# Kernel optimization log

Measured on AMD Instinct MI355X. Metric: run time of the kernel, lower is better.

The kernel has to match this reference:

```python
import jax, jax.numpy as jnp
import numpy as np

H = 16  # n_head

def _rms_norm(x):
    eps = jnp.asarray(jnp.finfo(x.dtype).eps, x.dtype)
    ms = jnp.mean(jnp.square(x), axis=-1, keepdims=True)
    return x * jax.lax.rsqrt(ms + eps)

def _interp(x, pos):
    # x: [B,T,H,Dh]; pos: [B,T,H,Dh] float positions along axis 1
    T = x.shape[1]
    pos_floor = jnp.floor(pos)
    pos0 = jnp.clip(pos_floor, 0, T - 1).astype(jnp.int32)
    pos1 = jnp.clip(pos0 + 1, 0, T - 1)
    frac = pos - pos_floor
    x0 = jnp.take_along_axis(x, pos0, axis=1)
    x1 = jnp.take_along_axis(x, pos1, axis=1)
    return x0 + (x1 - x0) * frac

def setup_inputs() -> dict:
    key = jax.random.key(0)
    ks = jax.random.split(key, 5)
    B, T, D = 4, 4096, 2048
    x = jax.random.normal(ks[0], (B, T, D), dtype=jnp.float32)
    scale = 0.02
    Wq = jax.random.normal(ks[1], (D, D), dtype=jnp.float32) * scale
    Wk = jax.random.normal(ks[2], (D, D), dtype=jnp.float32) * scale
    Wsq = jax.random.normal(ks[3], (D, D), dtype=jnp.float32) * scale
    Wsk = jax.random.normal(ks[4], (D, D), dtype=jnp.float32) * scale
    return {"x": x, "Wq": Wq, "Wk": Wk, "Wsq": Wsq, "Wsk": Wsk}

def reference(x, Wq, Wk, Wsq, Wsk):
    B, T, D = x.shape
    Dh = D // H
    # projections (Linear with weight [out,in]: y = x @ W.T)
    q = _rms_norm((x @ Wq.T).reshape(B, T, H, Dh))
    k = _rms_norm((x @ Wk.T).reshape(B, T, H, Dh))
    sq = jax.nn.softplus(x @ Wsq.T).reshape(B, T, H, Dh)
    sk = jax.nn.softplus(x @ Wsk.T).reshape(B, T, H, Dh)
    t_idx = jnp.arange(T, dtype=x.dtype).reshape(1, T, 1, 1)
    posq = jnp.minimum(jnp.maximum(t_idx - sq, 0.0), t_idx)
    posk = jnp.minimum(jnp.maximum(t_idx - sk, 0.0), t_idx)
    q_def = _interp(q, posq)
    k_def = _interp(k, posk)
    return (q_def * k_def).reshape(B, T, D)
```

## Files before the change

kernel.cpp:

```cpp
#include <hip/hip_runtime.h>

typedef unsigned short u16;
typedef __bf16 bf16x8 __attribute__((ext_vector_type(8)));
typedef unsigned short u16x8 __attribute__((ext_vector_type(8)));
typedef unsigned short u16x4 __attribute__((ext_vector_type(4)));
typedef float f32x4 __attribute__((ext_vector_type(4)));

#define K_DIM 2048
#define BM 128
#define BN 128
#define BK 32

#define GLL16(g, l) __builtin_amdgcn_global_load_lds( \
    (const __attribute__((address_space(1))) void*)(g), \
    (__attribute__((address_space(3))) void*)(l), 16, 0, 0)

__device__ __forceinline__ u16 f2bf(float f) {
    unsigned int u = __builtin_bit_cast(unsigned int, f);
    u = (u + 0x7fffu + ((u >> 16) & 1u)) >> 16;
    return (u16)u;
}
__device__ __forceinline__ float bf2f(u16 h) {
    unsigned int u = ((unsigned int)h) << 16;
    return __builtin_bit_cast(float, u);
}
__device__ __forceinline__ float softplus_f(float v) {
    return fmaxf(v, 0.0f) + log1pf(expf(-fabsf(v)));
}

__global__ void pack_kernel(const float* __restrict__ src, u16* __restrict__ dst, int n4) {
    int i = blockIdx.x * blockDim.x + threadIdx.x;
    if (i >= n4) return;
    float4 v = ((const float4*)src)[i];
    u16x4 o;
    o[0] = f2bf(v.x); o[1] = f2bf(v.y); o[2] = f2bf(v.z); o[3] = f2bf(v.w);
    ((u16x4*)dst)[i] = o;
}

__global__ void pack4_kernel(const float* __restrict__ s0, const float* __restrict__ s1,
                             const float* __restrict__ s2, const float* __restrict__ s3,
                             u16* __restrict__ dst) {
    int i = blockIdx.x * blockDim.x + threadIdx.x;
    const float* src = (blockIdx.y == 0) ? s0 : (blockIdx.y == 1) ? s1
                     : (blockIdx.y == 2) ? s2 : s3;
    float4 v = ((const float4*)src)[i];
    u16x4 o;
    o[0] = f2bf(v.x); o[1] = f2bf(v.y); o[2] = f2bf(v.z); o[3] = f2bf(v.w);
    ((u16x4*)(dst + (size_t)blockIdx.y * 4194304))[i] = o;
}

__global__ __launch_bounds__(256) void gemm_fused(
    const u16* __restrict__ xb, const u16* __restrict__ wb,
    u16* __restrict__ qb, u16* __restrict__ kb,
    u16* __restrict__ sqb, u16* __restrict__ skb)
{
    __shared__ u16 Als[BM * BK];
    __shared__ u16 Bls[BM * BK];
    __shared__ float ss[BM];

    const int tid  = threadIdx.x;
    const int lane = tid & 63;
    const int wave = tid >> 6;
    const int wm = wave >> 1;
    const int wn = wave & 1;
    const int gm0 = blockIdx.y * BM;
    const int gn0 = blockIdx.x * BN;

    const int r0 = tid >> 2;
    const int qs = ((tid & 3) - ((tid >> 3) & 3)) & 3;
    const int kc = qs * 8;
    const u16* gA0 = xb + (size_t)(gm0 + r0) * K_DIM + kc;
    const u16* gA1 = gA0 + (size_t)64 * K_DIM;
    const u16* gB0 = wb + (size_t)(gn0 + r0) * K_DIM + kc;
    const u16* gB1 = gB0 + (size_t)64 * K_DIM;
    char* lA0 = (char*)Als + wave * 1024;
    char* lA1 = (char*)Als + 4096 + wave * 1024;
    char* lB0 = (char*)Bls + wave * 1024;
    char* lB1 = (char*)Bls + 4096 + wave * 1024;

    f32x4 acc[4][4] = {};

    const int mr = lane & 15;
    const int q  = lane >> 4;
    const int s  = (q + (mr >> 1)) & 3;
    const int fragoff = mr * 32 + s * 8;

    for (int kt = 0; kt < K_DIM / BK; ++kt) {
        GLL16(gA0, lA0); GLL16(gA1, lA1);
        GLL16(gB0, lB0); GLL16(gB1, lB1);
        gA0 += BK; gA1 += BK; gB0 += BK; gB1 += BK;
        __syncthreads();

        bf16x8 a[4], b[4];
#pragma unroll
        for (int i = 0; i < 4; ++i)
            a[i] = __builtin_bit_cast(bf16x8, *(const u16x8*)&Als[(wm * 4 + i) * 512 + fragoff]);
#pragma unroll
        for (int j = 0; j < 4; ++j)
            b[j] = __builtin_bit_cast(bf16x8, *(const u16x8*)&Bls[(wn * 4 + j) * 512 + fragoff]);
#pragma unroll
        for (int i = 0; i < 4; ++i)
#pragma unroll
            for (int j = 0; j < 4; ++j)
                acc[i][j] = __builtin_amdgcn_mfma_f32_16x16x32_bf16(a[i], b[j], acc[i][j], 0, 0, 0);
        __syncthreads();
    }

    const int which = gn0 >> 11;
    if (tid < BM) ss[tid] = 0.0f;
    __syncthreads();

    const int mbase = wm * 64 + (lane >> 4) * 4;
    const int col0  = (gn0 & 2047) + wn * 64 + (lane & 15);

    if (which < 2) {
#pragma unroll
        for (int i = 0; i < 4; ++i) {
#pragma unroll
            for (int r = 0; r < 4; ++r) {
                float sv = acc[i][0][r] * acc[i][0][r] + acc[i][1][r] * acc[i][1][r]
                         + acc[i][2][r] * acc[i][2][r] + acc[i][3][r] * acc[i][3][r];
                sv += __shfl_xor(sv, 1, 64);
                sv += __shfl_xor(sv, 2, 64);
                sv += __shfl_xor(sv, 4, 64);
                sv += __shfl_xor(sv, 8, 64);
                if ((lane & 15) == 0) atomicAdd(&ss[mbase + i * 16 + r], sv);
            }
        }
        __syncthreads();
    }

    u16* ob = (which == 0) ? qb : (which == 1) ? kb : (which == 2) ? sqb : skb;
#pragma unroll
    for (int i = 0; i < 4; ++i) {
#pragma unroll
        for (int r = 0; r < 4; ++r) {
            int m = mbase + i * 16 + r;
            size_t rowbase = (size_t)(gm0 + m) * 2048;
            float scale = 1.0f;
            if (which < 2)
                scale = rsqrtf(ss[m] * (1.0f / 128.0f) + 1.1920929e-07f);
#pragma unroll
            for (int j = 0; j < 4; ++j) {
                float v = acc[i][j][r];
                v = (which < 2) ? v * scale : softplus_f(v);
                ob[rowbase + col0 + j * 16] = f2bf(v);
            }
        }
    }
}

__global__ void interp_mul(const u16* __restrict__ qb, const u16* __restrict__ kb,
                           const u16* __restrict__ sqb, const u16* __restrict__ skb,
                           float* __restrict__ out)
{
    size_t base = ((size_t)blockIdx.x * 256 + threadIdx.x) * 8;
    int c0 = (int)(base & 2047);
    size_t bt = base >> 11;
    int t = (int)(bt & 4095);
    float tf = (float)t;
    size_t rb = (base >> 23) << 23;

    u16x8 sqv8 = *(const u16x8*)&sqb[base];
    u16x8 skv8 = *(const u16x8*)&skb[base];

    float o[8];
#pragma unroll
    for (int e = 0; e < 8; ++e) {
        float sqv = bf2f(sqv8[e]);
        float skv = bf2f(skv8[e]);
        float pq = fminf(fmaxf(tf - sqv, 0.0f), tf);
        float pk = fminf(fmaxf(tf - skv, 0.0f), tf);
        float pqf = floorf(pq), pkf = floorf(pk);
        int q0i = (int)pqf, k0i = (int)pkf;
        int q1i = min(q0i + 1, 4095), k1i = min(k0i + 1, 4095);
        float fq = pq - pqf, fk = pk - pkf;
        size_t oo = rb + (size_t)(c0 + e);
        float q0 = bf2f(qb[oo + ((size_t)q0i << 11)]);
        float q1 = bf2f(qb[oo + ((size_t)q1i << 11)]);
        float k0 = bf2f(kb[oo + ((size_t)k0i << 11)]);
        float k1 = bf2f(kb[oo + ((size_t)k1i << 11)]);
        float qd = q0 + (q1 - q0) * fq;
        float kd = k0 + (k1 - k0) * fk;
        o[e] = qd * kd;
    }
    float4 lo = make_float4(o[0], o[1], o[2], o[3]);
    float4 hi = make_float4(o[4], o[5], o[6], o[7]);
    float4* op = (float4*)&out[base];
    op[0] = lo;
    op[1] = hi;
}

extern "C" void kernel_launch(void* const* d_in, const int* in_sizes, int n_in,
                              void* d_out, int out_size, void* d_ws, size_t ws_size,
                              hipStream_t stream) {
    const float* x   = (const float*)d_in[0];
    const float* Wq  = (const float*)d_in[1];
    const float* Wk  = (const float*)d_in[2];
    const float* Wsq = (const float*)d_in[3];
    const float* Wsk = (const float*)d_in[4];
    float* out = (float*)d_out;

    const size_t NEED = 369098752;
    if (ws_size < NEED) return;
    char* ws = (char*)d_ws;
    u16* xb  = (u16*)(ws);
    u16* wb  = (u16*)(ws + 67108864);
    u16* qb  = (u16*)(ws + 100663296);
    u16* kb  = (u16*)(ws + 167772160);
    u16* sqb = (u16*)(ws + 234881024);
    u16* skb = (u16*)(ws + 301989888);

    pack_kernel<<<32768, 256, 0, stream>>>(x, xb, 8388608);
    dim3 wgrid(4096, 4);
    pack4_kernel<<<wgrid, 256, 0, stream>>>(Wq, Wk, Wsq, Wsk, wb);

    dim3 ggrid(64, 128);
    gemm_fused<<<ggrid, 256, 0, stream>>>(xb, wb, qb, kb, sqb, skb);

    interp_mul<<<16384, 256, 0, stream>>>(qb, kb, sqb, skb, out);
}
```

Before: 1.201 ms.

## Rewrite GEMM as 256x256 tile, 8-wave, double-buffered pipeline with phased MFMA scheduling

The fused projection GEMM moves from 128x128 tiles with 4 waves and a single-buffered BK=32 loop to 256x256 tiles with 8 waves. It double-buffers 64-wide K slices in LDS and issues the global-to-LDS loads in halves interleaved with MFMA phases. Explicit sched barriers, s_barrier, s_setprio and vmcnt waits overlap memory traffic with matrix math and raise data reuse per tile. In exchange it uses much more LDS and accumulator registers, and each block's RMS-norm reduction now spans two heads in the shared buffer.

```diff
diff --git a/kernel.cpp b/kernel.cpp
--- a/kernel.cpp
+++ b/kernel.cpp
@@ -7,13 +7,17 @@
 typedef float f32x4 __attribute__((ext_vector_type(4)));
 
 #define K_DIM 2048
-#define BM 128
-#define BN 128
-#define BK 32
 
 #define GLL16(g, l) __builtin_amdgcn_global_load_lds( \
     (const __attribute__((address_space(1))) void*)(g), \
     (__attribute__((address_space(3))) void*)(l), 16, 0, 0)
+
+#define SB()  __builtin_amdgcn_sched_barrier(0)
+#define BAR() __builtin_amdgcn_s_barrier()
+#define PH_PRE()  do { SB(); BAR(); SB(); } while (0)
+#define PH_END()  do { SB(); BAR(); SB(); } while (0)
+#define PH_END_V4() do { SB(); asm volatile("s_waitcnt vmcnt(4)"); SB(); BAR(); SB(); } while (0)
+#define MFMA_(av, bv, cc) (cc) = __builtin_amdgcn_mfma_f32_16x16x32_bf16((av), (bv), (cc), 0, 0, 0)
 
 __device__ __forceinline__ u16 f2bf(float f) {
     unsigned int u = __builtin_bit_cast(unsigned int, f);
@@ -49,73 +53,210 @@
     ((u16x4*)(dst + (size_t)blockIdx.y * 4194304))[i] = o;
 }
 
-__global__ __launch_bounds__(256) void gemm_fused(
+__global__ __launch_bounds__(512, 2) void gemm_fused(
     const u16* __restrict__ xb, const u16* __restrict__ wb,
     u16* __restrict__ qb, u16* __restrict__ kb,
     u16* __restrict__ sqb, u16* __restrict__ skb)
 {
-    __shared__ u16 Als[BM * BK];
-    __shared__ u16 Bls[BM * BK];
-    __shared__ float ss[BM];
+    __shared__ __align__(16) u16 Als[32768];
+    __shared__ __align__(16) u16 Bls[32768];
+    __shared__ float ss[512];
 
     const int tid  = threadIdx.x;
     const int lane = tid & 63;
     const int wave = tid >> 6;
-    const int wm = wave >> 1;
-    const int wn = wave & 1;
-    const int gm0 = blockIdx.y * BM;
-    const int gn0 = blockIdx.x * BN;
-
-    const int r0 = tid >> 2;
-    const int qs = ((tid & 3) - ((tid >> 3) & 3)) & 3;
-    const int kc = qs * 8;
-    const u16* gA0 = xb + (size_t)(gm0 + r0) * K_DIM + kc;
-    const u16* gA1 = gA0 + (size_t)64 * K_DIM;
-    const u16* gB0 = wb + (size_t)(gn0 + r0) * K_DIM + kc;
-    const u16* gB1 = gB0 + (size_t)64 * K_DIM;
-    char* lA0 = (char*)Als + wave * 1024;
-    char* lA1 = (char*)Als + 4096 + wave * 1024;
-    char* lB0 = (char*)Bls + wave * 1024;
-    char* lB1 = (char*)Bls + 4096 + wave * 1024;
-
-    f32x4 acc[4][4] = {};
-
-    const int mr = lane & 15;
-    const int q  = lane >> 4;
-    const int s  = (q + (mr >> 1)) & 3;
-    const int fragoff = mr * 32 + s * 8;
-
-    for (int kt = 0; kt < K_DIM / BK; ++kt) {
-        GLL16(gA0, lA0); GLL16(gA1, lA1);
-        GLL16(gB0, lB0); GLL16(gB1, lB1);
-        gA0 += BK; gA1 += BK; gB0 += BK; gB1 += BK;
-        __syncthreads();
-
-        bf16x8 a[4], b[4];
-#pragma unroll
-        for (int i = 0; i < 4; ++i)
-            a[i] = __builtin_bit_cast(bf16x8, *(const u16x8*)&Als[(wm * 4 + i) * 512 + fragoff]);
-#pragma unroll
-        for (int j = 0; j < 4; ++j)
-            b[j] = __builtin_bit_cast(bf16x8, *(const u16x8*)&Bls[(wn * 4 + j) * 512 + fragoff]);
-#pragma unroll
-        for (int i = 0; i < 4; ++i)
-#pragma unroll
-            for (int j = 0; j < 4; ++j)
-                acc[i][j] = __builtin_amdgcn_mfma_f32_16x16x32_bf16(a[i], b[j], acc[i][j], 0, 0, 0);
-        __syncthreads();
+    const int wm   = wave >> 2;
+    const int wn   = wave & 3;
+    const int gm0  = blockIdx.y * 256;
+    const int gn0  = blockIdx.x * 256;
+
+    const int q8 = (((lane & 3) - ((lane >> 3) & 3)) & 3) * 8;
+    const int sB = wave * 512;
+    const u16* pa0 = xb + (size_t)(gm0 + wave * 16 + (lane >> 2)) * K_DIM + q8;
+    const u16* pb0 = wb + (size_t)(gn0 + wave * 16 + (lane >> 2)) * K_DIM + q8;
+    const size_t SRC1 = (size_t)128 * K_DIM;
+
+    const int mr  = lane & 15;
+    const int srd = ((lane >> 4) + (mr >> 1)) & 3;
+    const int fro = mr * 32 + srd * 8;
+    const int aRB = wm * 8 * 512 + fro;
+    const int bRB = wn * 4 * 512 + fro;
+
+    f32x4 acc[8][4] = {};
+
+#define LDA(buf, i, ks) __builtin_bit_cast(bf16x8, *(const u16x8*)&Als[(buf)*16384 + (ks)*8192 + aRB + (i)*512])
+#define LDB(buf, j, ks) __builtin_bit_cast(bf16x8, *(const u16x8*)&Bls[(buf)*16384 + (ks)*8192 + bRB + (j)*512])
+#define STAGE_A(coff, dbase) do { \
+    GLL16(pa0 + (coff),          &Als[(dbase) + sB]); \
+    GLL16(pa0 + (coff) + SRC1,   &Als[(dbase) + sB + 4096]); \
+    GLL16(pa0 + (coff) + 32,     &Als[(dbase) + sB + 8192]); \
+    GLL16(pa0 + (coff) + SRC1 + 32, &Als[(dbase) + sB + 12288]); } while (0)
+#define STAGE_B(coff, dbase) do { \
+    GLL16(pb0 + (coff),          &Bls[(dbase) + sB]); \
+    GLL16(pb0 + (coff) + SRC1,   &Bls[(dbase) + sB + 4096]); \
+    GLL16(pb0 + (coff) + 32,     &Bls[(dbase) + sB + 8192]); \
+    GLL16(pb0 + (coff) + SRC1 + 32, &Bls[(dbase) + sB + 12288]); } while (0)
+#define STAGE_A_H0(coff, dbase) do { \
+    GLL16(pa0 + (coff),        &Als[(dbase) + sB]); \
+    GLL16(pa0 + (coff) + SRC1, &Als[(dbase) + sB + 4096]); } while (0)
+#define STAGE_A_H1(coff, dbase) do { \
+    GLL16(pa0 + (coff) + 32,        &Als[(dbase) + sB + 8192]); \
+    GLL16(pa0 + (coff) + SRC1 + 32, &Als[(dbase) + sB + 12288]); } while (0)
+#define STAGE_B_H0(coff, dbase) do { \
+    GLL16(pb0 + (coff),        &Bls[(dbase) + sB]); \
+    GLL16(pb0 + (coff) + SRC1, &Bls[(dbase) + sB + 4096]); } while (0)
+#define STAGE_B_H1(coff, dbase) do { \
+    GLL16(pb0 + (coff) + 32,        &Bls[(dbase) + sB + 8192]); \
+    GLL16(pb0 + (coff) + SRC1 + 32, &Bls[(dbase) + sB + 12288]); } while (0)
+
+    STAGE_A(0, 0);
+    STAGE_B(0, 0);
+    STAGE_B(64, 16384);
+    __syncthreads();
+
+    for (int it = 0; it < 16; ++it) {
+        bf16x8 aF[4][2], b01[2][2], b23[2][2];
+
+#pragma unroll
+        for (int i = 0; i < 4; ++i) { aF[i][0] = LDA(0, i, 0); aF[i][1] = LDA(0, i, 1); }
+#pragma unroll
+        for (int j = 0; j < 2; ++j) { b01[j][0] = LDB(0, j, 0); b01[j][1] = LDB(0, j, 1); }
+        STAGE_A_H0(64, 16384);
+        PH_PRE();
+        __builtin_amdgcn_s_setprio(1);
+#pragma unroll
+        for (int i = 0; i < 4; ++i) MFMA_(aF[i][0], b01[0][0], acc[i][0]);
+#pragma unroll
+        for (int i = 0; i < 4; ++i) MFMA_(aF[i][0], b01[1][0], acc[i][1]);
+#pragma unroll
+        for (int i = 0; i < 4; ++i) MFMA_(aF[i][1], b01[0][1], acc[i][0]);
+#pragma unroll
+        for (int i = 0; i < 4; ++i) MFMA_(aF[i][1], b01[1][1], acc[i][1]);
+        __builtin_amdgcn_s_setprio(0);
+        PH_END();
+
+#pragma unroll
+        for (int j = 0; j < 2; ++j) { b23[j][0] = LDB(0, j + 2, 0); b23[j][1] = LDB(0, j + 2, 1); }
+        STAGE_A_H1(64, 16384);
+        PH_PRE();
+        __builtin_amdgcn_s_setprio(1);
+#pragma unroll
+        for (int i = 0; i < 4; ++i) MFMA_(aF[i][0], b23[0][0], acc[i][2]);
+#pragma unroll
+        for (int i = 0; i < 4; ++i) MFMA_(aF[i][0], b23[1][0], acc[i][3]);
+#pragma unroll
+        for (int i = 0; i < 4; ++i) MFMA_(aF[i][1], b23[0][1], acc[i][2]);
+#pragma unroll
+        for (int i = 0; i < 4; ++i) MFMA_(aF[i][1], b23[1][1], acc[i][3]);
+        __builtin_amdgcn_s_setprio(0);
+        PH_END();
+
+#pragma unroll
+        for (int i = 0; i < 4; ++i) { aF[i][0] = LDA(0, i + 4, 0); aF[i][1] = LDA(0, i + 4, 1); }
+        STAGE_B_H0(128, 0);
+        PH_PRE();
+        __builtin_amdgcn_s_setprio(1);
+#pragma unroll
+        for (int i = 0; i < 4; ++i) MFMA_(aF[i][0], b23[0][0], acc[4 + i][2]);
+#pragma unroll
+        for (int i = 0; i < 4; ++i) MFMA_(aF[i][0], b23[1][0], acc[4 + i][3]);
+#pragma unroll
+        for (int i = 0; i < 4; ++i) MFMA_(aF[i][1], b23[0][1], acc[4 + i][2]);
+#pragma unroll
+        for (int i = 0; i < 4; ++i) MFMA_(aF[i][1], b23[1][1], acc[4 + i][3]);
+        __builtin_amdgcn_s_setprio(0);
+        PH_END();
+
+        STAGE_B_H1(128, 0);
+        PH_PRE();
+        __builtin_amdgcn_s_setprio(1);
+#pragma unroll
+        for (int i = 0; i < 4; ++i) MFMA_(aF[i][0], b01[0][0], acc[4 + i][0]);
+#pragma unroll
+        for (int i = 0; i < 4; ++i) MFMA_(aF[i][0], b01[1][0], acc[4 + i][1]);
+#pragma unroll
+        for (int i = 0; i < 4; ++i) MFMA_(aF[i][1], b01[0][1], acc[4 + i][0]);
+#pragma unroll
+        for (int i = 0; i < 4; ++i) MFMA_(aF[i][1], b01[1][1], acc[4 + i][1]);
+        __builtin_amdgcn_s_setprio(0);
+        PH_END_V4();
+
+#pragma unroll
+        for (int i = 0; i < 4; ++i) { aF[i][0] = LDA(1, i, 0); aF[i][1] = LDA(1, i, 1); }
+#pragma unroll
+        for (int j = 0; j < 2; ++j) { b01[j][0] = LDB(1, j, 0); b01[j][1] = LDB(1, j, 1); }
+        STAGE_A_H0(128, 0);
+        PH_PRE();
+        __builtin_amdgcn_s_setprio(1);
+#pragma unroll
+        for (int i = 0; i < 4; ++i) MFMA_(aF[i][0], b01[0][0], acc[i][0]);
+#pragma unroll
+        for (int i = 0; i < 4; ++i) MFMA_(aF[i][0], b01[1][0], acc[i][1]);
+#pragma unroll
+        for (int i = 0; i < 4; ++i) MFMA_(aF[i][1], b01[0][1], acc[i][0]);
+#pragma unroll
+        for (int i = 0; i < 4; ++i) MFMA_(aF[i][1], b01[1][1], acc[i][1]);
+        __builtin_amdgcn_s_setprio(0);
+        PH_END();
+
+#pragma unroll
+        for (int j = 0; j < 2; ++j) { b23[j][0] = LDB(1, j + 2, 0); b23[j][1] = LDB(1, j + 2, 1); }
+        STAGE_A_H1(128, 0);
+        PH_PRE();
+        __builtin_amdgcn_s_setprio(1);
+#pragma unroll
+        for (int i = 0; i < 4; ++i) MFMA_(aF[i][0], b23[0][0], acc[i][2]);
+#pragma unroll
+        for (int i = 0; i < 4; ++i) MFMA_(aF[i][0], b23[1][0], acc[i][3]);
+#pragma unroll
+        for (int i = 0; i < 4; ++i) MFMA_(aF[i][1], b23[0][1], acc[i][2]);
+#pragma unroll
+        for (int i = 0; i < 4; ++i) MFMA_(aF[i][1], b23[1][1], acc[i][3]);
+        __builtin_amdgcn_s_setprio(0);
+        PH_END();
+
+#pragma unroll
+        for (int i = 0; i < 4; ++i) { aF[i][0] = LDA(1, i + 4, 0); aF[i][1] = LDA(1, i + 4, 1); }
+        STAGE_B_H0(192, 16384);
+        PH_PRE();
+        __builtin_amdgcn_s_setprio(1);
+#pragma unroll
+        for (int i = 0; i < 4; ++i) MFMA_(aF[i][0], b23[0][0], acc[4 + i][2]);
+#pragma unroll
+        for (int i = 0; i < 4; ++i) MFMA_(aF[i][0], b23[1][0], acc[4 + i][3]);
+#pragma unroll
+        for (int i = 0; i < 4; ++i) MFMA_(aF[i][1], b23[0][1], acc[4 + i][2]);
+#pragma unroll
+        for (int i = 0; i < 4; ++i) MFMA_(aF[i][1], b23[1][1], acc[4 + i][3]);
+        __builtin_amdgcn_s_setprio(0);
+        PH_END();
+
+        STAGE_B_H1(192, 16384);
+        PH_PRE();
+        __builtin_amdgcn_s_setprio(1);
+#pragma unroll
+        for (int i = 0; i < 4; ++i) MFMA_(aF[i][0], b01[0][0], acc[4 + i][0]);
+#pragma unroll
+        for (int i = 0; i < 4; ++i) MFMA_(aF[i][0], b01[1][0], acc[4 + i][1]);
+#pragma unroll
+        for (int i = 0; i < 4; ++i) MFMA_(aF[i][1], b01[0][1], acc[4 + i][0]);
+#pragma unroll
+        for (int i = 0; i < 4; ++i) MFMA_(aF[i][1], b01[1][1], acc[4 + i][1]);
+        __builtin_amdgcn_s_setprio(0);
+        PH_END_V4();
+
+        pa0 += 128; pb0 += 128;
     }
+    asm volatile("s_waitcnt vmcnt(0)" ::: "memory");
 
     const int which = gn0 >> 11;
-    if (tid < BM) ss[tid] = 0.0f;
+    ss[tid] = 0.0f;
     __syncthreads();
 
-    const int mbase = wm * 64 + (lane >> 4) * 4;
-    const int col0  = (gn0 & 2047) + wn * 64 + (lane & 15);
-
+    const int h = wn >> 1;
     if (which < 2) {
 #pragma unroll
-        for (int i = 0; i < 4; ++i) {
+        for (int i = 0; i < 8; ++i) {
 #pragma unroll
             for (int r = 0; r < 4; ++r) {
                 float sv = acc[i][0][r] * acc[i][0][r] + acc[i][1][r] * acc[i][1][r]
@@ -124,22 +265,24 @@
                 sv += __shfl_xor(sv, 2, 64);
                 sv += __shfl_xor(sv, 4, 64);
                 sv += __shfl_xor(sv, 8, 64);
-                if ((lane & 15) == 0) atomicAdd(&ss[mbase + i * 16 + r], sv);
+                if ((lane & 15) == 0)
+                    atomicAdd(&ss[h * 256 + wm * 128 + i * 16 + (lane >> 4) * 4 + r], sv);
             }
         }
         __syncthreads();
     }
 
     u16* ob = (which == 0) ? qb : (which == 1) ? kb : (which == 2) ? sqb : skb;
-#pragma unroll
-    for (int i = 0; i < 4; ++i) {
+    const int col0 = (gn0 & 2047) + wn * 64 + (lane & 15);
+#pragma unroll
+    for (int i = 0; i < 8; ++i) {
 #pragma unroll
         for (int r = 0; r < 4; ++r) {
-            int m = mbase + i * 16 + r;
-            size_t rowbase = (size_t)(gm0 + m) * 2048;
+            const int m = wm * 128 + i * 16 + (lane >> 4) * 4 + r;
+            const size_t rowbase = (size_t)(gm0 + m) * 2048;
             float scale = 1.0f;
             if (which < 2)
-                scale = rsqrtf(ss[m] * (1.0f / 128.0f) + 1.1920929e-07f);
+                scale = rsqrtf(ss[h * 256 + m] * (1.0f / 128.0f) + 1.1920929e-07f);
 #pragma unroll
             for (int j = 0; j < 4; ++j) {
                 float v = acc[i][j][r];
@@ -184,11 +327,9 @@
         float kd = k0 + (k1 - k0) * fk;
         o[e] = qd * kd;
     }
-    float4 lo = make_float4(o[0], o[1], o[2], o[3]);
-    float4 hi = make_float4(o[4], o[5], o[6], o[7]);
     float4* op = (float4*)&out[base];
-    op[0] = lo;
-    op[1] = hi;
+    op[0] = make_float4(o[0], o[1], o[2], o[3]);
+    op[1] = make_float4(o[4], o[5], o[6], o[7]);
 }
 
 extern "C" void kernel_launch(void* const* d_in, const int* in_sizes, int n_in,
@@ -215,8 +356,8 @@
     dim3 wgrid(4096, 4);
     pack4_kernel<<<wgrid, 256, 0, stream>>>(Wq, Wk, Wsq, Wsk, wb);
 
-    dim3 ggrid(64, 128);
-    gemm_fused<<<ggrid, 256, 0, stream>>>(xb, wb, qb, kb, sqb, skb);
+    dim3 ggrid(32, 64);
+    gemm_fused<<<ggrid, 512, 0, stream>>>(xb, wb, qb, kb, sqb, skb);
 
     interp_mul<<<16384, 256, 0, stream>>>(qb, kb, sqb, skb, out);
 }
```

Result: slower. 1.476 ms (+22.9%).
